# Kernel optimization log

Hardware: AMD Instinct MI355X
Metric: run time of the kernel (lower is better)

Reference implementation:

```python
import jax, jax.numpy as jnp
import numpy as np

D_MODEL = 1024
NUM_HEADS = 16
D_HEAD = 64
D_MLP = 4096
SEQ = 2048
BATCH = 4
NEG_BIG = 1e10


def setup_inputs() -> dict:
    key = jax.random.key(0)
    ks = jax.random.split(key, 10)
    s = 1.0 / np.sqrt(D_MODEL)
    return {
        "x": jax.random.normal(ks[0], (BATCH, SEQ, D_MODEL), dtype=jnp.float32),
        "W_K": jax.random.normal(ks[1], (NUM_HEADS, D_HEAD, D_MODEL), dtype=jnp.float32) * s,
        "W_Q": jax.random.normal(ks[2], (NUM_HEADS, D_HEAD, D_MODEL), dtype=jnp.float32) * s,
        "W_V": jax.random.normal(ks[3], (NUM_HEADS, D_HEAD, D_MODEL), dtype=jnp.float32) * s,
        "W_O": jax.random.normal(ks[4], (D_MODEL, D_HEAD * NUM_HEADS), dtype=jnp.float32) * s,
        "W_in": jax.random.normal(ks[5], (D_MLP, D_MODEL), dtype=jnp.float32) * s,
        "b_in": jnp.zeros((D_MLP,), dtype=jnp.float32),
        "W_out": jax.random.normal(ks[6], (D_MODEL, D_MLP), dtype=jnp.float32) * s,
        "b_out": jnp.zeros((D_MODEL,), dtype=jnp.float32),
    }


def _block(x, W_K, W_Q, W_V, W_O, W_in, b_in, W_out, b_out):
    seq = x.shape[1]
    # Attention
    k = jnp.einsum("ihd,bpd->biph", W_K, x)
    q = jnp.einsum("ihd,bpd->biph", W_Q, x)
    v = jnp.einsum("ihd,bpd->biph", W_V, x)
    scores = jnp.einsum("biph,biqh->biqp", k, q)  # [b, i, q(query), p(key)]
    mask = jnp.tril(jnp.ones((seq, seq), dtype=x.dtype))  # causal: key p <= query q
    scores = scores * mask - NEG_BIG * (1.0 - mask)
    attn = jax.nn.softmax(scores / np.sqrt(D_HEAD), axis=-1)
    z = jnp.einsum("biph,biqp->biqh", v, attn)  # [b, heads, q, d_head]
    z_flat = jnp.transpose(z, (0, 2, 1, 3)).reshape(z.shape[0], seq, -1)  # b q (i h)
    attn_out = jnp.einsum("df,bqf->bqd", W_O, z_flat)
    x = x + attn_out
    # MLP
    h = jnp.einsum("md,bpd->bpm", W_in, x) + b_in
    h = jax.nn.gelu(h, approximate=False)
    mlp_out = jnp.einsum("dm,bpm->bpd", W_out, h) + b_out
    return x + mlp_out


def reference(x, W_K, W_Q, W_V, W_O, W_in, b_in, W_out, b_out):
    return _block(x, W_K, W_Q, W_V, W_O, W_in, b_in, W_out, b_out)
```

## Files before the change

kernel.cpp:

```cpp
#include <hip/hip_runtime.h>
#include <hip/hip_bf16.h>

typedef __bf16 bf16;
typedef __bf16 bf16x8 __attribute__((ext_vector_type(8)));
typedef __bf16 bf16x4 __attribute__((ext_vector_type(4)));
typedef float  f32x4  __attribute__((ext_vector_type(4)));

#define MFMA(a,b,c) __builtin_amdgcn_mfma_f32_16x16x32_bf16(a,b,c,0,0,0)
#define EXP2F(x) __builtin_amdgcn_exp2f(x)

__device__ __forceinline__ void gload16(const void* g, void* l) {
  __builtin_amdgcn_global_load_lds((__attribute__((address_space(1))) void*)(g),
                                   (__attribute__((address_space(3))) void*)(l), 16, 0, 0);
}

struct CastSegs {
  const float* src[7];
  bf16* dst[7];
  int cum[8];
};

__global__ void cast_multi(CastSegs s) {
  int i = blockIdx.x * 256 + threadIdx.x;
  if (i >= s.cum[7]) return;
  int k = 0;
  #pragma unroll
  for (int j = 1; j < 7; ++j) if (i >= s.cum[j]) k = j;
  int off = i - s.cum[k];
  const float4* p = (const float4*)s.src[k];
  float4 a = p[2*off], b = p[2*off+1];
  bf16x8 v;
  v[0]=(bf16)a.x; v[1]=(bf16)a.y; v[2]=(bf16)a.z; v[3]=(bf16)a.w;
  v[4]=(bf16)b.x; v[5]=(bf16)b.y; v[6]=(bf16)b.z; v[7]=(bf16)b.w;
  *(bf16x8*)(s.dst[k] + (size_t)8*off) = v;
}

__device__ __forceinline__ float gelu_t(float s) {
  float u = s * (0.7978845608f + 0.0356774081f * s * s);
  return s / (1.0f + EXP2F(-2.885390082f * u));
}

#define LGKM0_FENCE() { asm volatile("s_waitcnt lgkmcnt(0)" ::: "memory"); \
                        __builtin_amdgcn_sched_barrier(0); }

#define LDA_PH(MI2) { _Pragma("unroll") for (int i = 0; i < 4; i++) { \
    af[i][0] = *(const bf16x8*)(lds + ab + ((((MI2)<<2)+i) << 11) + rdswz); \
    af[i][1] = *(const bf16x8*)(lds + ab + ((((MI2)<<2)+i) << 11) + 1024 + rdswz); } }

#define LDB_PH(NI2) { _Pragma("unroll") for (int n = 0; n < 2; n++) { \
    bfr[((NI2)<<1)+n][0] = *(const bf16x8*)(lds + bb + (((((NI2)<<1)+n)) << 11) + rdswz); \
    bfr[((NI2)<<1)+n][1] = *(const bf16x8*)(lds + bb + (((((NI2)<<1)+n)) << 11) + 1024 + rdswz); } }

#define MM_PH(MI2, NI2) { __builtin_amdgcn_s_setprio(1); \
    _Pragma("unroll") for (int i = 0; i < 4; i++) \
      _Pragma("unroll") for (int n = 0; n < 2; n++) { \
        acc[((MI2)<<2)+i][((NI2)<<1)+n] = MFMA(af[i][0], bfr[((NI2)<<1)+n][0], acc[((MI2)<<2)+i][((NI2)<<1)+n]); \
        acc[((MI2)<<2)+i][((NI2)<<1)+n] = MFMA(af[i][1], bfr[((NI2)<<1)+n][1], acc[((MI2)<<2)+i][((NI2)<<1)+n]); } \
    __builtin_amdgcn_s_setprio(0); }

#define GTILE(CUR, S1, S2, VM) { \
    const int ab = ((CUR) << 16) + (wm << 14); \
    const int bb = ((CUR) << 16) + 32768 + (wn << 13); \
    LDA_PH(0); LDB_PH(0); \
    if (S1) STG(sA, (CUR)^1, 0, 1, t + 1); \
    asm volatile("s_waitcnt lgkmcnt(8)" ::: "memory"); \
    __builtin_amdgcn_s_barrier(); LGKM0_FENCE(); \
    MM_PH(0, 0); \
    LDB_PH(1); \
    if (S2) STG(sB, (CUR), 1, 0, t + 2); \
    __builtin_amdgcn_s_barrier(); LGKM0_FENCE(); \
    MM_PH(0, 1); \
    LDA_PH(1); \
    if (S2) STG(sB, (CUR), 1, 1, t + 2); \
    __builtin_amdgcn_s_barrier(); LGKM0_FENCE(); \
    MM_PH(1, 0); \
    if (S2) STG(sA, (CUR), 0, 0, t + 2); \
    MM_PH(1, 1); \
    asm volatile("s_waitcnt vmcnt(" #VM ")" ::: "memory"); \
    __builtin_amdgcn_s_barrier(); \
    __builtin_amdgcn_sched_barrier(0); }

template<int EPI>
__global__ __launch_bounds__(512, 2) void gemm256(
    const bf16* __restrict__ A, const bf16* __restrict__ B,
    float* __restrict__ outf, bf16* __restrict__ outb,
    const float* __restrict__ add, const float* __restrict__ bias,
    int M, int N, int K, int gx)
{
  __shared__ __attribute__((aligned(128))) char lds[131072];
  const int tid = threadIdx.x;
  const int w = tid >> 6, l = tid & 63, lg = l >> 4, li = l & 15;
  const int wm = w >> 2, wn = w & 3;

  const int nwg = gridDim.x, orig = blockIdx.x;
  const int q = nwg >> 3, r = nwg & 7;
  const int xcd = orig & 7, pos = orig >> 3;
  const int wg = (xcd < r ? xcd*(q+1) : r*(q+1) + (xcd-r)*q) + pos;
  const int m0 = (wg / gx) << 8, n0 = (wg % gx) << 8;

  const int NT = K >> 6;

  const int srow = ((tid >> 7) << 4) + ((tid >> 2) & 15);
  const int scol = (((tid >> 6) & 1) << 5) + (((tid & 3) << 3) ^ (((tid >> 5) & 1) << 4));
  const bf16* sA = A + (size_t)(m0 + srow) * K + scol;
  const bf16* sB = B + (size_t)(n0 + srow) * K + scol;
  char* const myl = lds + (w << 10);

  auto STG = [&](const bf16* s0, int buf, int isB, int h, int tt) {
    const bf16* g = s0 + ((size_t)(h << 7)) * K + ((size_t)tt << 6);
    char* lb = myl + (buf << 16) + (isB << 15) + (h << 14);
    gload16(g, lb);
    gload16(g + ((size_t)K << 6), lb + 8192);
  };

  const int rdswz = (li << 6) + ((lg << 4) ^ ((li & 8) << 2));

  f32x4 acc[8][4] = {};
  bf16x8 af[4][2], bfr[4][2];

  STG(sB, 0, 1, 0, 0); STG(sB, 0, 1, 1, 0); STG(sA, 0, 0, 0, 0); STG(sA, 0, 0, 1, 0);
  asm volatile("s_waitcnt vmcnt(4)" ::: "memory");
  STG(sB, 1, 1, 0, 1); STG(sB, 1, 1, 1, 1); STG(sA, 1, 0, 0, 1);
  asm volatile("s_waitcnt vmcnt(6)" ::: "memory");
  __builtin_amdgcn_s_barrier();
  __builtin_amdgcn_sched_barrier(0);

  int t = 0;
  for (int tt = 0; tt + 3 < NT; tt += 2) {
    t = tt;     GTILE(0, 1, 1, 6);
    t = tt + 1; GTILE(1, 1, 1, 6);
  }
  t = NT - 2; GTILE(0, 1, 0, 0);
  t = NT - 1; GTILE(1, 0, 0, 0);

  #pragma unroll
  for (int mi = 0; mi < 8; mi++) {
    const int row = m0 + (wm << 7) + (mi << 4) + (lg << 2);
    #pragma unroll
    for (int ni = 0; ni < 4; ni++) {
      const int col = n0 + (wn << 6) + (ni << 4) + li;
      #pragma unroll
      for (int r2 = 0; r2 < 4; r2++) {
        const size_t idx = (size_t)(row + r2) * N + col;
        float v = acc[mi][ni][r2];
        if (EPI == 0) {
          outb[idx] = (bf16)v;
        } else if (EPI == 1) {
          float s = v + add[idx];
          outf[idx] = s; outb[idx] = (bf16)s;
        } else if (EPI == 2) {
          outb[idx] = (bf16)gelu_t(v + bias[col]);
        } else {
          outf[idx] = v + bias[col] + add[idx];
        }
      }
    }
  }
}

#define N_LDA2(BMI) { _Pragma("unroll") for (int i = 0; i < 2; i++) { \
    af[i][0] = *(const bf16x8*)(lds + abase + (((BMI)+i) << 11) + rdswz); \
    af[i][1] = *(const bf16x8*)(lds + abase + (((BMI)+i) << 11) + 1024 + rdswz); } }

#define N_LDB2(BNI) { _Pragma("unroll") for (int n = 0; n < 2; n++) { \
    bfr[(BNI)+n][0] = *(const bf16x8*)(lds + bbase + (((BNI)+n) << 11) + rdswz); \
    bfr[(BNI)+n][1] = *(const bf16x8*)(lds + bbase + (((BNI)+n) << 11) + 1024 + rdswz); } }

#define N_MMQ(MB, NB) { __builtin_amdgcn_s_setprio(1); \
    _Pragma("unroll") for (int i = 0; i < 2; i++) \
      _Pragma("unroll") for (int n = 0; n < 2; n++) { \
        acc[((MB)<<1)+i][((NB)<<1)+n] = MFMA(af[i][0], bfr[((NB)<<1)+n][0], acc[((MB)<<1)+i][((NB)<<1)+n]); \
        acc[((MB)<<1)+i][((NB)<<1)+n] = MFMA(af[i][1], bfr[((NB)<<1)+n][1], acc[((MB)<<1)+i][((NB)<<1)+n]); } \
    __builtin_amdgcn_s_setprio(0); }

#define NTILE(CUR, S1, S2, VM) { \
    const int abase = (CUR) * 49152 + ((wm >> 1) << 14) + ((wm & 1) << 13); \
    const int bbase = (CUR) * 49152 + 32768 + (wn << 13); \
    N_LDA2(0); N_LDB2(0); \
    if (S1) STA((CUR)^1, 1, t + 1); \
    __builtin_amdgcn_s_barrier(); LGKM0_FENCE(); \
    N_MMQ(0, 0); \
    N_LDB2(2); \
    if (S2) STB((CUR), 0, t + 2); \
    __builtin_amdgcn_s_barrier(); LGKM0_FENCE(); \
    N_MMQ(0, 1); \
    N_LDA2(2); \
    if (S2) STB((CUR), 1, t + 2); \
    __builtin_amdgcn_s_barrier(); LGKM0_FENCE(); \
    N_MMQ(1, 0); \
    if (S2) STA((CUR), 0, t + 2); \
    N_MMQ(1, 1); \
    asm volatile("s_waitcnt vmcnt(" #VM ")" ::: "memory"); \
    __builtin_amdgcn_s_barrier(); \
    __builtin_amdgcn_sched_barrier(0); }

template<int EPI>
__global__ __launch_bounds__(512, 2) void gemm128n(
    const bf16* __restrict__ A, const bf16* __restrict__ B,
    float* __restrict__ outf, bf16* __restrict__ outb,
    const float* __restrict__ add, const float* __restrict__ bias,
    bf16* __restrict__ vtb,
    int M, int N, int K, int gx)
{
  __shared__ __attribute__((aligned(128))) char lds[98304];
  const int tid = threadIdx.x;
  const int w = tid >> 6, l = tid & 63, lg = l >> 4, li = l & 15;
  const int wm = w >> 1, wn = w & 1;

  const int nwg = gridDim.x, orig = blockIdx.x;
  const int q = nwg >> 3, r = nwg & 7;
  const int xcd = orig & 7, pos = orig >> 3;
  const int wg = (xcd < r ? xcd*(q+1) : r*(q+1) + (xcd-r)*q) + pos;
  const int m0 = (wg / gx) << 8, n0 = (wg % gx) << 7;

  const int NT = K >> 6;

  const int srow = ((tid >> 7) << 4) + ((tid >> 2) & 15);
  const int scol = (((tid >> 6) & 1) << 5) + (((tid & 3) << 3) ^ (((tid >> 5) & 1) << 4));
  const bf16* sA = A + (size_t)(m0 + srow) * K + scol;
  const bf16* sB = B + (size_t)(n0 + srow) * K + scol;
  char* const myl = lds + (w << 10);

  auto STA = [&](int buf, int h, int tt) {
    const bf16* g = sA + ((size_t)(h << 7)) * K + ((size_t)tt << 6);
    char* lb = myl + buf * 49152 + (h << 14);
    gload16(g, lb);
    gload16(g + ((size_t)K << 6), lb + 8192);
  };
  auto STB = [&](int buf, int h, int tt) {
    const bf16* g = sB + ((size_t)(h << 6)) * K + ((size_t)tt << 6);
    gload16(g, myl + buf * 49152 + 32768 + (h << 13));
  };

  const int rdswz = (li << 6) + ((lg << 4) ^ ((li & 8) << 2));

  f32x4 acc[4][4] = {};
  bf16x8 af[2][2], bfr[4][2];

  STB(0, 0, 0); STB(0, 1, 0); STA(0, 0, 0); STA(0, 1, 0);
  STB(1, 0, 1); STB(1, 1, 1); STA(1, 0, 1);
  asm volatile("s_waitcnt vmcnt(4)" ::: "memory");
  __builtin_amdgcn_s_barrier();
  __builtin_amdgcn_sched_barrier(0);

  int t = 0;
  for (int tt = 0; tt + 3 < NT; tt += 2) {
    t = tt;     NTILE(0, 1, 1, 4);
    t = tt + 1; NTILE(1, 1, 1, 4);
  }
  t = NT - 2; NTILE(0, 1, 0, 0);
  t = NT - 1; NTILE(1, 0, 0, 0);

  if (EPI == 0 && n0 >= 2048) {
    #pragma unroll
    for (int mi = 0; mi < 4; mi++) {
      const int row = m0 + (wm << 6) + (mi << 4) + (lg << 2);
      const int p = row & 2047;
      const size_t bhb = (size_t)((row >> 11) << 4);
      #pragma unroll
      for (int ni = 0; ni < 4; ni++) {
        const int col = n0 + (wn << 6) + (ni << 4) + li;
        const int hh = (col >> 6) & 15, dd = col & 63;
        bf16x4 pk;
        pk[0] = (bf16)acc[mi][ni][0]; pk[1] = (bf16)acc[mi][ni][1];
        pk[2] = (bf16)acc[mi][ni][2]; pk[3] = (bf16)acc[mi][ni][3];
        *(bf16x4*)(vtb + ((bhb + hh) * 64 + dd) * 2048 + p) = pk;
      }
    }
    return;
  }

  #pragma unroll
  for (int mi = 0; mi < 4; mi++) {
    const int row = m0 + (wm << 6) + (mi << 4) + (lg << 2);
    #pragma unroll
    for (int ni = 0; ni < 4; ni++) {
      const int col = n0 + (wn << 6) + (ni << 4) + li;
      #pragma unroll
      for (int r2 = 0; r2 < 4; r2++) {
        const size_t idx = (size_t)(row + r2) * N + col;
        float v = acc[mi][ni][r2];
        if (EPI == 0) {
          outb[idx] = (bf16)v;
        } else if (EPI == 1) {
          float s = v + add[idx];
          outf[idx] = s; outb[idx] = (bf16)s;
        } else if (EPI == 2) {
          outb[idx] = (bf16)gelu_t(v + bias[col]);
        } else {
          outf[idx] = v + bias[col] + add[idx];
        }
      }
    }
  }
}

__global__ __launch_bounds__(256) void attn_kernel(const bf16* __restrict__ qkv,
                                                   const bf16* __restrict__ vt,
                                                   bf16* __restrict__ z)
{
  __shared__ bf16 Ksh[2][64*64];
  __shared__ bf16 Vsh[2][64*64];
  __shared__ bf16 Pl[4*16*64];

  const int tid = threadIdx.x;
  const int w = tid >> 6, l = tid & 63, lg = l >> 4, li = l & 15;
  const int orig = blockIdx.x;
  const int xcd = orig & 7, sub = orig >> 3;
  const int bh = (xcd << 3) + (sub >> 4);
  const int pr = sub & 15;
  const int h = bh & 15, b = bh >> 4;
  const size_t tb = (size_t)b * 2048;

  const int srow = tid >> 3, sc = tid & 7;
  const bf16* Kg = qkv + (tb + srow) * 3072 + 1024 + (h << 6) + ((sc ^ (srow & 7)) << 3);
  const bf16* Vg = vt + ((size_t)bh * 64 + srow) * 2048 + ((sc ^ (srow & 7)) << 3);

  char* pw = (char*)Pl + (w << 11) + li * 128;
  const int psw = (li & 3) << 5;

  for (int hf = 0; hf < 2; ++hf) {
    const int qt = hf ? pr : (31 - pr);
    const int qw = (qt << 6) + (w << 4);

    const bf16* Qp = qkv + (tb + qw + li) * 3072 + (h << 6);
    bf16x8 qa0 = *(const bf16x8*)(Qp + (lg << 3));
    bf16x8 qa1 = *(const bf16x8*)(Qp + 32 + (lg << 3));
    #pragma unroll
    for (int e = 0; e < 8; e++) {
      qa0[e] = (bf16)((float)qa0[e] * 0.1803368801f);
      qa1[e] = (bf16)((float)qa1[e] * 0.1803368801f);
    }

    f32x4 zacc[4] = {};
    float mR = -1e30f, lS = 0.f;
    const int nkt = qt + 1;

    gload16(Kg,                   (bf16*)Ksh[0] + (w << 9));
    gload16(Kg + (size_t)32*3072, (bf16*)Ksh[0] + 2048 + (w << 9));
    gload16(Vg,                   (bf16*)Vsh[0] + (w << 9));
    gload16(Vg + (size_t)32*2048, (bf16*)Vsh[0] + 2048 + (w << 9));
    __syncthreads();

    for (int kt = 0; kt < nkt; ++kt) {
      const int cur = kt & 1;
      const int pb = kt << 6;

      if (kt + 1 < nkt) {
        const int nb = cur ^ 1;
        const size_t ko = (size_t)(pb + 64) * 3072;
        gload16(Kg + ko,                   (bf16*)Ksh[nb] + (w << 9));
        gload16(Kg + ko + (size_t)32*3072, (bf16*)Ksh[nb] + 2048 + (w << 9));
        gload16(Vg + pb + 64,                   (bf16*)Vsh[nb] + (w << 9));
        gload16(Vg + pb + 64 + (size_t)32*2048, (bf16*)Vsh[nb] + 2048 + (w << 9));
      }

      f32x4 s[4];
      __builtin_amdgcn_s_setprio(1);
      #pragma unroll
      for (int sub2 = 0; sub2 < 4; ++sub2) {
        const char* kr = (const char*)Ksh[cur] + ((sub2 << 4) + li) * 128;
        const int c0 = (lg ^ (li & 7)) << 4;
        bf16x8 kb0 = *(const bf16x8*)(kr + c0);
        bf16x8 kb1 = *(const bf16x8*)(kr + (c0 ^ 64));
        f32x4 a2 = {};
        a2 = MFMA(kb0, qa0, a2);
        a2 = MFMA(kb1, qa1, a2);
        s[sub2] = a2;
      }
      __builtin_amdgcn_s_setprio(0);

      if (pb + 63 > qw) {
        #pragma unroll
        for (int sub2 = 0; sub2 < 4; ++sub2)
          #pragma unroll
          for (int r = 0; r < 4; ++r)
            if (pb + (sub2 << 4) + (lg << 2) + r > qw + li) s[sub2][r] = -1e30f;
      }

      f32x4 m4;
      #pragma unroll
      for (int r = 0; r < 4; ++r)
        m4[r] = fmaxf(fmaxf(s[0][r], s[1][r]), fmaxf(s[2][r], s[3][r]));
      float mx = fmaxf(fmaxf(m4[0], m4[1]), fmaxf(m4[2], m4[3]));
      mx = fmaxf(mx, __shfl_xor(mx, 16));
      mx = fmaxf(mx, __shfl_xor(mx, 32));

      float mn = mR;
      if (!__all(mx <= mR + 11.5f)) {
        mn = fmaxf(mR, mx);
        float c = EXP2F(mR - mn);
        mR = mn;
        lS *= c;
        float cr0 = __shfl(c, (lg << 2) + 0);
        float cr1 = __shfl(c, (lg << 2) + 1);
        float cr2 = __shfl(c, (lg << 2) + 2);
        float cr3 = __shfl(c, (lg << 2) + 3);
        #pragma unroll
        for (int d = 0; d < 4; ++d) {
          zacc[d][0] *= cr0; zacc[d][1] *= cr1;
          zacc[d][2] *= cr2; zacc[d][3] *= cr3;
        }
      }

      f32x4 p[4];
      #pragma unroll
      for (int sub2 = 0; sub2 < 4; ++sub2)
        #pragma unroll
        for (int r = 0; r < 4; ++r)
          p[sub2][r] = EXP2F(s[sub2][r] - mn);
      f32x4 t4 = p[0] + p[1] + p[2] + p[3];
      lS += (t4[0] + t4[1]) + (t4[2] + t4[3]);

      #pragma unroll
      for (int sub2 = 0; sub2 < 4; ++sub2) {
        bf16x4 pk;
        pk[0] = (bf16)p[sub2][0]; pk[1] = (bf16)p[sub2][1];
        pk[2] = (bf16)p[sub2][2]; pk[3] = (bf16)p[sub2][3];
        *(bf16x4*)(pw + (((sub2 << 5) + (lg << 3)) ^ psw)) = pk;
      }

      __builtin_amdgcn_s_setprio(1);
      #pragma unroll
      for (int kc = 0; kc < 2; ++kc) {
        bf16x8 pa = *(const bf16x8*)(pw + (((kc << 6) + (lg << 4)) ^ psw));
        #pragma unroll
        for (int d = 0; d < 4; ++d) {
          const char* vr = (const char*)Vsh[cur] + ((d << 4) + li) * 128;
          bf16x8 vb = *(const bf16x8*)(vr + ((((kc << 2) + lg) ^ (li & 7)) << 4));
          zacc[d] = MFMA(pa, vb, zacc[d]);
        }
      }
      __builtin_amdgcn_s_setprio(0);

      __syncthreads();
    }

    lS += __shfl_xor(lS, 16);
    lS += __shfl_xor(lS, 32);

    float rls[4];
    #pragma unroll
    for (int r = 0; r < 4; ++r) rls[r] = 1.0f / __shfl(lS, (lg << 2) + r);
    bf16* zp = z + (tb + qw) * 1024 + (h << 6);
    #pragma unroll
    for (int d = 0; d < 4; ++d)
      #pragma unroll
      for (int r = 0; r < 4; ++r)
        zp[(size_t)((lg << 2) + r) * 1024 + (d << 4) + li] = (bf16)(zacc[d][r] * rls[r]);
  }
}

extern "C" void kernel_launch(void* const* d_in, const int* in_sizes, int n_in,
                              void* d_out, int out_size, void* d_ws, size_t ws_size,
                              hipStream_t stream)
{
  const float* x     = (const float*)d_in[0];
  const float* W_K   = (const float*)d_in[1];
  const float* W_Q   = (const float*)d_in[2];
  const float* W_V   = (const float*)d_in[3];
  const float* W_O   = (const float*)d_in[4];
  const float* W_in  = (const float*)d_in[5];
  const float* b_in  = (const float*)d_in[6];
  const float* W_out = (const float*)d_in[7];
  const float* b_out = (const float*)d_in[8];
  float* out = (float*)d_out;

  char* ws = (char*)d_ws;
  bf16*  xb   = (bf16*)ws;  ws += (size_t)8192*1024*2;
  bf16*  wqkv = (bf16*)ws;  ws += (size_t)3072*1024*2;
  bf16*  wo   = (bf16*)ws;  ws += (size_t)1024*1024*2;
  bf16*  win  = (bf16*)ws;  ws += (size_t)4096*1024*2;
  bf16*  wout = (bf16*)ws;  ws += (size_t)1024*4096*2;
  bf16*  qkv  = (bf16*)ws;  ws += (size_t)8192*3072*2;
  bf16*  zb   = (bf16*)ws;  ws += (size_t)8192*1024*2;
  float* x1f  = (float*)ws; ws += (size_t)8192*1024*4;
  bf16*  x1b  = (bf16*)ws;  ws += (size_t)8192*1024*2;
  bf16*  hb   = (bf16*)ws;
  bf16*  vtb  = hb;

  CastSegs cs;
  const float* srcs[7] = { x, W_Q, W_K, W_V, W_O, W_in, W_out };
  bf16* dsts[7] = { xb, wqkv, wqkv + 1024*1024, wqkv + 2048*1024, wo, win, wout };
  int n8s[7] = { 1048576, 131072, 131072, 131072, 131072, 524288, 524288 };
  int cum = 0;
  for (int i = 0; i < 7; ++i) { cs.src[i] = srcs[i]; cs.dst[i] = dsts[i]; cs.cum[i] = cum; cum += n8s[i]; }
  cs.cum[7] = cum;
  cast_multi<<<dim3((cum + 255) / 256), dim3(256), 0, stream>>>(cs);

  gemm128n<0><<<dim3(768), 512, 0, stream>>>(xb, wqkv, nullptr, qkv, nullptr, nullptr, vtb, 8192, 3072, 1024, 24);
  attn_kernel<<<dim3(1024), 256, 0, stream>>>(qkv, vtb, zb);
  gemm128n<1><<<dim3(256), 512, 0, stream>>>(zb, wo, x1f, x1b, x, nullptr, nullptr, 8192, 1024, 1024, 8);
  gemm256<2><<<dim3(512), 512, 0, stream>>>(x1b, win, nullptr, hb, nullptr, b_in, 8192, 4096, 1024, 16);
  gemm128n<3><<<dim3(256), 512, 0, stream>>>(hb, wout, out, nullptr, x1f, b_out, nullptr, 8192, 1024, 4096, 8);
}
```

Measured before the change: 310.4 us.

## Use 128-tile GEMM for MLP up-projection and defer softmax max shuffles

Drops the 256x256-tile gemm256 kernel. The MLP input projection with GELU now runs on the existing gemm128n kernel over 1024 workgroups, which trades per-tile data reuse for more workgroups and better load balance across CUs. In the attention softmax, the cross-lane max reduction is now done only when some lane's local max exceeds the running max threshold. This removes two shuffles per tile in the common case.

```diff
diff --git a/kernel.cpp b/kernel.cpp
--- a/kernel.cpp
+++ b/kernel.cpp
@@ -42,121 +42,6 @@
 
 #define LGKM0_FENCE() { asm volatile("s_waitcnt lgkmcnt(0)" ::: "memory"); \
                         __builtin_amdgcn_sched_barrier(0); }
-
-#define LDA_PH(MI2) { _Pragma("unroll") for (int i = 0; i < 4; i++) { \
-    af[i][0] = *(const bf16x8*)(lds + ab + ((((MI2)<<2)+i) << 11) + rdswz); \
-    af[i][1] = *(const bf16x8*)(lds + ab + ((((MI2)<<2)+i) << 11) + 1024 + rdswz); } }
-
-#define LDB_PH(NI2) { _Pragma("unroll") for (int n = 0; n < 2; n++) { \
-    bfr[((NI2)<<1)+n][0] = *(const bf16x8*)(lds + bb + (((((NI2)<<1)+n)) << 11) + rdswz); \
-    bfr[((NI2)<<1)+n][1] = *(const bf16x8*)(lds + bb + (((((NI2)<<1)+n)) << 11) + 1024 + rdswz); } }
-
-#define MM_PH(MI2, NI2) { __builtin_amdgcn_s_setprio(1); \
-    _Pragma("unroll") for (int i = 0; i < 4; i++) \
-      _Pragma("unroll") for (int n = 0; n < 2; n++) { \
-        acc[((MI2)<<2)+i][((NI2)<<1)+n] = MFMA(af[i][0], bfr[((NI2)<<1)+n][0], acc[((MI2)<<2)+i][((NI2)<<1)+n]); \
-        acc[((MI2)<<2)+i][((NI2)<<1)+n] = MFMA(af[i][1], bfr[((NI2)<<1)+n][1], acc[((MI2)<<2)+i][((NI2)<<1)+n]); } \
-    __builtin_amdgcn_s_setprio(0); }
-
-#define GTILE(CUR, S1, S2, VM) { \
-    const int ab = ((CUR) << 16) + (wm << 14); \
-    const int bb = ((CUR) << 16) + 32768 + (wn << 13); \
-    LDA_PH(0); LDB_PH(0); \
-    if (S1) STG(sA, (CUR)^1, 0, 1, t + 1); \
-    asm volatile("s_waitcnt lgkmcnt(8)" ::: "memory"); \
-    __builtin_amdgcn_s_barrier(); LGKM0_FENCE(); \
-    MM_PH(0, 0); \
-    LDB_PH(1); \
-    if (S2) STG(sB, (CUR), 1, 0, t + 2); \
-    __builtin_amdgcn_s_barrier(); LGKM0_FENCE(); \
-    MM_PH(0, 1); \
-    LDA_PH(1); \
-    if (S2) STG(sB, (CUR), 1, 1, t + 2); \
-    __builtin_amdgcn_s_barrier(); LGKM0_FENCE(); \
-    MM_PH(1, 0); \
-    if (S2) STG(sA, (CUR), 0, 0, t + 2); \
-    MM_PH(1, 1); \
-    asm volatile("s_waitcnt vmcnt(" #VM ")" ::: "memory"); \
-    __builtin_amdgcn_s_barrier(); \
-    __builtin_amdgcn_sched_barrier(0); }
-
-template<int EPI>
-__global__ __launch_bounds__(512, 2) void gemm256(
-    const bf16* __restrict__ A, const bf16* __restrict__ B,
-    float* __restrict__ outf, bf16* __restrict__ outb,
-    const float* __restrict__ add, const float* __restrict__ bias,
-    int M, int N, int K, int gx)
-{
-  __shared__ __attribute__((aligned(128))) char lds[131072];
-  const int tid = threadIdx.x;
-  const int w = tid >> 6, l = tid & 63, lg = l >> 4, li = l & 15;
-  const int wm = w >> 2, wn = w & 3;
-
-  const int nwg = gridDim.x, orig = blockIdx.x;
-  const int q = nwg >> 3, r = nwg & 7;
-  const int xcd = orig & 7, pos = orig >> 3;
-  const int wg = (xcd < r ? xcd*(q+1) : r*(q+1) + (xcd-r)*q) + pos;
-  const int m0 = (wg / gx) << 8, n0 = (wg % gx) << 8;
-
-  const int NT = K >> 6;
-
-  const int srow = ((tid >> 7) << 4) + ((tid >> 2) & 15);
-  const int scol = (((tid >> 6) & 1) << 5) + (((tid & 3) << 3) ^ (((tid >> 5) & 1) << 4));
-  const bf16* sA = A + (size_t)(m0 + srow) * K + scol;
-  const bf16* sB = B + (size_t)(n0 + srow) * K + scol;
-  char* const myl = lds + (w << 10);
-
-  auto STG = [&](const bf16* s0, int buf, int isB, int h, int tt) {
-    const bf16* g = s0 + ((size_t)(h << 7)) * K + ((size_t)tt << 6);
-    char* lb = myl + (buf << 16) + (isB << 15) + (h << 14);
-    gload16(g, lb);
-    gload16(g + ((size_t)K << 6), lb + 8192);
-  };
-
-  const int rdswz = (li << 6) + ((lg << 4) ^ ((li & 8) << 2));
-
-  f32x4 acc[8][4] = {};
-  bf16x8 af[4][2], bfr[4][2];
-
-  STG(sB, 0, 1, 0, 0); STG(sB, 0, 1, 1, 0); STG(sA, 0, 0, 0, 0); STG(sA, 0, 0, 1, 0);
-  asm volatile("s_waitcnt vmcnt(4)" ::: "memory");
-  STG(sB, 1, 1, 0, 1); STG(sB, 1, 1, 1, 1); STG(sA, 1, 0, 0, 1);
-  asm volatile("s_waitcnt vmcnt(6)" ::: "memory");
-  __builtin_amdgcn_s_barrier();
-  __builtin_amdgcn_sched_barrier(0);
-
-  int t = 0;
-  for (int tt = 0; tt + 3 < NT; tt += 2) {
-    t = tt;     GTILE(0, 1, 1, 6);
-    t = tt + 1; GTILE(1, 1, 1, 6);
-  }
-  t = NT - 2; GTILE(0, 1, 0, 0);
-  t = NT - 1; GTILE(1, 0, 0, 0);
-
-  #pragma unroll
-  for (int mi = 0; mi < 8; mi++) {
-    const int row = m0 + (wm << 7) + (mi << 4) + (lg << 2);
-    #pragma unroll
-    for (int ni = 0; ni < 4; ni++) {
-      const int col = n0 + (wn << 6) + (ni << 4) + li;
-      #pragma unroll
-      for (int r2 = 0; r2 < 4; r2++) {
-        const size_t idx = (size_t)(row + r2) * N + col;
-        float v = acc[mi][ni][r2];
-        if (EPI == 0) {
-          outb[idx] = (bf16)v;
-        } else if (EPI == 1) {
-          float s = v + add[idx];
-          outf[idx] = s; outb[idx] = (bf16)s;
-        } else if (EPI == 2) {
-          outb[idx] = (bf16)gelu_t(v + bias[col]);
-        } else {
-          outf[idx] = v + bias[col] + add[idx];
-        }
-      }
-    }
-  }
-}
 
 #define N_LDA2(BMI) { _Pragma("unroll") for (int i = 0; i < 2; i++) { \
     af[i][0] = *(const bf16x8*)(lds + abase + (((BMI)+i) << 11) + rdswz); \
@@ -382,12 +267,12 @@
       #pragma unroll
       for (int r = 0; r < 4; ++r)
         m4[r] = fmaxf(fmaxf(s[0][r], s[1][r]), fmaxf(s[2][r], s[3][r]));
-      float mx = fmaxf(fmaxf(m4[0], m4[1]), fmaxf(m4[2], m4[3]));
-      mx = fmaxf(mx, __shfl_xor(mx, 16));
-      mx = fmaxf(mx, __shfl_xor(mx, 32));
+      float lmx = fmaxf(fmaxf(m4[0], m4[1]), fmaxf(m4[2], m4[3]));
 
       float mn = mR;
-      if (!__all(mx <= mR + 11.5f)) {
+      if (!__all(lmx <= mR + 11.5f)) {
+        float mx = fmaxf(lmx, __shfl_xor(lmx, 16));
+        mx = fmaxf(mx, __shfl_xor(mx, 32));
         mn = fmaxf(mR, mx);
         float c = EXP2F(mR - mn);
         mR = mn;
@@ -491,6 +376,6 @@
   gemm128n<0><<<dim3(768), 512, 0, stream>>>(xb, wqkv, nullptr, qkv, nullptr, nullptr, vtb, 8192, 3072, 1024, 24);
   attn_kernel<<<dim3(1024), 256, 0, stream>>>(qkv, vtb, zb);
   gemm128n<1><<<dim3(256), 512, 0, stream>>>(zb, wo, x1f, x1b, x, nullptr, nullptr, 8192, 1024, 1024, 8);
-  gemm256<2><<<dim3(512), 512, 0, stream>>>(x1b, win, nullptr, hb, nullptr, b_in, 8192, 4096, 1024, 16);
+  gemm128n<2><<<dim3(1024), 512, 0, stream>>>(x1b, win, nullptr, hb, nullptr, b_in, nullptr, 8192, 4096, 1024, 32);
   gemm128n<3><<<dim3(256), 512, 0, stream>>>(hb, wout, out, nullptr, x1f, b_out, nullptr, 8192, 1024, 4096, 8);
 }
```

Measured after the change: 321.3 us. 1.03x slower.

## Keep residual stream in bf16, drop fp32 residual buffer, defer softmax max shuffles

Applied to the files above, without the earlier changes.

The attention-output GEMM now adds the bf16 copy of x and writes only a bf16 residual, and the final GEMM reads that bf16 residual instead of an fp32 one. This removes the fp32 x1 write and its later read, cutting memory traffic. In exchange, residual precision drops to bf16, which adds error to the output. The softmax row-max cross-lane shuffles are also moved inside the rare rescale branch, and an unused V-transpose epilogue is added to gemm256 (never launched with EPI 0).

```diff
diff --git a/kernel.cpp b/kernel.cpp
--- a/kernel.cpp
+++ b/kernel.cpp
@@ -42,6 +42,7 @@
 
 #define LGKM0_FENCE() { asm volatile("s_waitcnt lgkmcnt(0)" ::: "memory"); \
                         __builtin_amdgcn_sched_barrier(0); }
+
 
 #define LDA_PH(MI2) { _Pragma("unroll") for (int i = 0; i < 4; i++) { \
     af[i][0] = *(const bf16x8*)(lds + ab + ((((MI2)<<2)+i) << 11) + rdswz); \
@@ -84,7 +85,8 @@
 __global__ __launch_bounds__(512, 2) void gemm256(
     const bf16* __restrict__ A, const bf16* __restrict__ B,
     float* __restrict__ outf, bf16* __restrict__ outb,
-    const float* __restrict__ add, const float* __restrict__ bias,
+    const bf16* __restrict__ addb, const float* __restrict__ bias,
+    bf16* __restrict__ vtb,
     int M, int N, int K, int gx)
 {
   __shared__ __attribute__((aligned(128))) char lds[131072];
@@ -133,6 +135,25 @@
   t = NT - 2; GTILE(0, 1, 0, 0);
   t = NT - 1; GTILE(1, 0, 0, 0);
 
+  if (EPI == 0 && n0 >= 2048) {
+    #pragma unroll
+    for (int mi = 0; mi < 8; mi++) {
+      const int row = m0 + (wm << 7) + (mi << 4) + (lg << 2);
+      const int p = row & 2047;
+      const size_t bhb = (size_t)((row >> 11) << 4);
+      #pragma unroll
+      for (int ni = 0; ni < 4; ni++) {
+        const int col = n0 + (wn << 6) + (ni << 4) + li;
+        const int hh = (col >> 6) & 15, dd = col & 63;
+        bf16x4 pk;
+        pk[0] = (bf16)acc[mi][ni][0]; pk[1] = (bf16)acc[mi][ni][1];
+        pk[2] = (bf16)acc[mi][ni][2]; pk[3] = (bf16)acc[mi][ni][3];
+        *(bf16x4*)(vtb + ((bhb + hh) * 64 + dd) * 2048 + p) = pk;
+      }
+    }
+    return;
+  }
+
   #pragma unroll
   for (int mi = 0; mi < 8; mi++) {
     const int row = m0 + (wm << 7) + (mi << 4) + (lg << 2);
@@ -146,12 +167,11 @@
         if (EPI == 0) {
           outb[idx] = (bf16)v;
         } else if (EPI == 1) {
-          float s = v + add[idx];
-          outf[idx] = s; outb[idx] = (bf16)s;
+          outb[idx] = (bf16)(v + (float)addb[idx]);
         } else if (EPI == 2) {
           outb[idx] = (bf16)gelu_t(v + bias[col]);
         } else {
-          outf[idx] = v + bias[col] + add[idx];
+          outf[idx] = v + bias[col] + (float)addb[idx];
         }
       }
     }
@@ -198,7 +218,7 @@
 __global__ __launch_bounds__(512, 2) void gemm128n(
     const bf16* __restrict__ A, const bf16* __restrict__ B,
     float* __restrict__ outf, bf16* __restrict__ outb,
-    const float* __restrict__ add, const float* __restrict__ bias,
+    const bf16* __restrict__ addb, const float* __restrict__ bias,
     bf16* __restrict__ vtb,
     int M, int N, int K, int gx)
 {
@@ -283,12 +303,11 @@
         if (EPI == 0) {
           outb[idx] = (bf16)v;
         } else if (EPI == 1) {
-          float s = v + add[idx];
-          outf[idx] = s; outb[idx] = (bf16)s;
+          outb[idx] = (bf16)(v + (float)addb[idx]);
         } else if (EPI == 2) {
           outb[idx] = (bf16)gelu_t(v + bias[col]);
         } else {
-          outf[idx] = v + bias[col] + add[idx];
+          outf[idx] = v + bias[col] + (float)addb[idx];
         }
       }
     }
@@ -382,12 +401,12 @@
       #pragma unroll
       for (int r = 0; r < 4; ++r)
         m4[r] = fmaxf(fmaxf(s[0][r], s[1][r]), fmaxf(s[2][r], s[3][r]));
-      float mx = fmaxf(fmaxf(m4[0], m4[1]), fmaxf(m4[2], m4[3]));
-      mx = fmaxf(mx, __shfl_xor(mx, 16));
-      mx = fmaxf(mx, __shfl_xor(mx, 32));
+      float lmx = fmaxf(fmaxf(m4[0], m4[1]), fmaxf(m4[2], m4[3]));
 
       float mn = mR;
-      if (!__all(mx <= mR + 11.5f)) {
+      if (!__all(lmx <= mR + 11.5f)) {
+        float mx = fmaxf(lmx, __shfl_xor(lmx, 16));
+        mx = fmaxf(mx, __shfl_xor(mx, 32));
         mn = fmaxf(mR, mx);
         float c = EXP2F(mR - mn);
         mR = mn;
@@ -474,7 +493,6 @@
   bf16*  wout = (bf16*)ws;  ws += (size_t)1024*4096*2;
   bf16*  qkv  = (bf16*)ws;  ws += (size_t)8192*3072*2;
   bf16*  zb   = (bf16*)ws;  ws += (size_t)8192*1024*2;
-  float* x1f  = (float*)ws; ws += (size_t)8192*1024*4;
   bf16*  x1b  = (bf16*)ws;  ws += (size_t)8192*1024*2;
   bf16*  hb   = (bf16*)ws;
   bf16*  vtb  = hb;
@@ -490,7 +508,7 @@
 
   gemm128n<0><<<dim3(768), 512, 0, stream>>>(xb, wqkv, nullptr, qkv, nullptr, nullptr, vtb, 8192, 3072, 1024, 24);
   attn_kernel<<<dim3(1024), 256, 0, stream>>>(qkv, vtb, zb);
-  gemm128n<1><<<dim3(256), 512, 0, stream>>>(zb, wo, x1f, x1b, x, nullptr, nullptr, 8192, 1024, 1024, 8);
-  gemm256<2><<<dim3(512), 512, 0, stream>>>(x1b, win, nullptr, hb, nullptr, b_in, 8192, 4096, 1024, 16);
-  gemm128n<3><<<dim3(256), 512, 0, stream>>>(hb, wout, out, nullptr, x1f, b_out, nullptr, 8192, 1024, 4096, 8);
-}
+  gemm128n<1><<<dim3(256), 512, 0, stream>>>(zb, wo, nullptr, x1b, xb, nullptr, nullptr, 8192, 1024, 1024, 8);
+  gemm256<2><<<dim3(512), 512, 0, stream>>>(x1b, win, nullptr, hb, nullptr, b_in, nullptr, 8192, 4096, 1024, 16);
+  gemm128n<3><<<dim3(256), 512, 0, stream>>>(hb, wout, out, nullptr, x1b, b_out, nullptr, 8192, 1024, 4096, 8);
+}
```

Measured after the change: 296.7 us. 1.05x faster.
